# Kernel tuning notes

Measured on AMD Instinct MI355X. Metric: run time of the kernel, lower is better.

Reference implementation:

```python
import jax, jax.numpy as jnp
import numpy as np
import math

B, S, E, H = 4, 2048, 512, 8
D = E // H

def setup_inputs() -> dict:
    key = jax.random.key(0)
    ks = jax.random.split(key, 12)
    inp = {
        'query': jax.random.normal(ks[0], (B, S, E), jnp.float32),
        'key': jax.random.normal(ks[1], (B, S, E), jnp.float32),
        'value': jax.random.normal(ks[2], (B, S, E), jnp.float32),
        'mask': jnp.ones((B, S), jnp.int32),
        'position_bias': jax.random.normal(ks[3], (H, S, S), jnp.float32) * 0.02,
        'Wq': jax.random.normal(ks[4], (E, E), jnp.float32) * 0.02,
        'bq': jnp.zeros((E,), jnp.float32),
        'Wk': jax.random.normal(ks[5], (E, E), jnp.float32) * 0.02,
        'bk': jnp.zeros((E,), jnp.float32),
        'Wv': jax.random.normal(ks[6], (E, E), jnp.float32) * 0.02,
        'bv': jnp.zeros((E,), jnp.float32),
        'Wo': jax.random.normal(ks[7], (E, E), jnp.float32) * 0.02,
        'bo': jnp.zeros((E,), jnp.float32),
    }
    return inp

def reference(query, key, value, mask, position_bias, Wq, bq, Wk, bk, Wv, bv, Wo, bo):
    scale = math.sqrt(D)
    # torch Linear: x @ W.T + b
    Q = (query @ Wq.T + bq).reshape(B, S, H, D).transpose(0, 2, 1, 3)  # bhsd
    K = (key @ Wk.T + bk).reshape(B, S, H, D).transpose(0, 2, 1, 3)
    V = (value @ Wv.T + bv).reshape(B, S, H, D).transpose(0, 2, 1, 3)
    scores = jnp.einsum('bhqd,bhkd->bhqk', Q, K) / scale
    scores = scores + position_bias[None]
    causal = jnp.triu(jnp.ones((S, S), bool), k=1)  # True above diagonal
    scores = jnp.where(causal[None, None], -jnp.inf, scores)
    scores = jnp.where(mask[:, None, None, :] == 0, -jnp.inf, scores)
    attn = jax.nn.softmax(scores, axis=-1)  # dropout is eval no-op
    ctx = jnp.einsum('bhqk,bhkd->bqhd', attn, V).reshape(B, S, E)
    out = ctx @ Wo.T + bo
    return out, attn
```

## Files before the change

### kernel.cpp

```cpp
#include <hip/hip_runtime.h>

typedef __attribute__((ext_vector_type(8))) __bf16 bf16x8;
typedef __attribute__((ext_vector_type(4))) float f32x4;
typedef __attribute__((ext_vector_type(4))) unsigned short u16x4;
typedef unsigned short u16;

#define OFF_QB   0L
#define OFF_KB   4194304L
#define OFF_VB   8388608L
#define OFF_WQ   12582912L
#define OFF_WK   12845056L
#define OFF_WV   13107200L
#define OFF_WO   13369344L
#define OFF_QS   13631488L
#define OFF_KS   17825792L
#define OFF_VT   22020096L
#define OFF_CTX  26214400L
#define WS_NEEDED_U16 30408704L

static __device__ __forceinline__ u16 f2bf(float f) {
  union { float f; unsigned u; } v; v.f = f;
  unsigned r = v.u + 0x7FFFu + ((v.u >> 16) & 1u);
  return (u16)(r >> 16);
}

static __device__ __forceinline__ f32x4 mfma16(bf16x8 a, bf16x8 b, f32x4 c) {
  return __builtin_amdgcn_mfma_f32_16x16x32_bf16(a, b, c, 0, 0, 0);
}

__global__ __launch_bounds__(256) void k_cvt(
    const float* __restrict__ q, const float* __restrict__ k, const float* __restrict__ v,
    const float* __restrict__ wq, const float* __restrict__ wk, const float* __restrict__ wv,
    const float* __restrict__ wo, u16* __restrict__ ws0) {
  long i = ((long)blockIdx.x * 256 + threadIdx.x) * 4;
  const float* src; u16* dst; long off;
  if (i < 12582912L) {
    int which = (int)(i >> 22); off = i & 4194303L;
    src = which == 0 ? q : which == 1 ? k : v;
    dst = ws0 + (long)which * 4194304L;
  } else {
    long j = i - 12582912L;
    int which = (int)(j >> 18); off = j & 262143L;
    src = which == 0 ? wq : which == 1 ? wk : which == 2 ? wv : wo;
    dst = ws0 + 12582912L + (long)which * 262144L;
  }
  float4 f = *(const float4*)(src + off);
  u16x4 o; o.x = f2bf(f.x); o.y = f2bf(f.y); o.z = f2bf(f.z); o.w = f2bf(f.w);
  *(u16x4*)(dst + off) = o;
}

__global__ __launch_bounds__(256) void k_proj_qk(
    const u16* __restrict__ ws0, const float* __restrict__ bq, const float* __restrict__ bk) {
  const int wv  = threadIdx.x >> 6;
  const int lane = threadIdx.x & 63;
  const int r16 = lane & 15, g8 = (lane >> 4) * 8, rq = (lane >> 4) * 4;
  const int t0 = blockIdx.x * 64 + wv * 16;
  const int e0 = blockIdx.y * 64;
  const int z  = blockIdx.z;
  const u16* xb = ws0 + (z == 0 ? OFF_QB : OFF_KB);
  const u16* wb = ws0 + (z == 0 ? OFF_WQ : OFF_WK);
  const float* bias = (z == 0) ? bq : bk;
  u16* dst = (u16*)ws0 + (z == 0 ? OFF_QS : OFF_KS);
  const float scl = (z == 0) ? 0.125f * 1.4426950408889634f : 1.0f;

  f32x4 acc[4] = {};
  const u16* arow = xb + (long)(t0 + r16) * 512 + g8;
  for (int f = 0; f < 512; f += 32) {
    bf16x8 a = *(const bf16x8*)(arow + f);
#pragma unroll
    for (int nt = 0; nt < 4; ++nt) {
      bf16x8 bfr = *(const bf16x8*)(wb + (long)(e0 + nt * 16 + r16) * 512 + f + g8);
      acc[nt] = mfma16(a, bfr, acc[nt]);
    }
  }
#pragma unroll
  for (int nt = 0; nt < 4; ++nt) {
    int e = e0 + nt * 16 + r16;
    float bb = bias[e];
    int h = e >> 6, d = e & 63;
#pragma unroll
    for (int r = 0; r < 4; ++r) {
      int t = t0 + rq + r;
      int b = t >> 11, s = t & 2047;
      float val = (acc[nt][r] + bb) * scl;
      dst[((long)(b * 8 + h) * 2048 + s) * 64 + d] = f2bf(val);
    }
  }
}

__global__ __launch_bounds__(256) void k_proj_v(
    const u16* __restrict__ ws0, const float* __restrict__ bv) {
  const int wv  = threadIdx.x >> 6;
  const int lane = threadIdx.x & 63;
  const int r16 = lane & 15, g8 = (lane >> 4) * 8, rq = (lane >> 4) * 4;
  const int e0 = blockIdx.x * 64 + wv * 16;
  const int t0 = blockIdx.y * 64;
  const u16* xb = ws0 + OFF_VB;
  const u16* wb = ws0 + OFF_WV;
  u16* vt = (u16*)ws0 + OFF_VT;

  f32x4 acc[4] = {};
  const u16* arow = wb + (long)(e0 + r16) * 512 + g8;
  for (int f = 0; f < 512; f += 32) {
    bf16x8 a = *(const bf16x8*)(arow + f);
#pragma unroll
    for (int nt = 0; nt < 4; ++nt) {
      bf16x8 bfr = *(const bf16x8*)(xb + (long)(t0 + nt * 16 + r16) * 512 + f + g8);
      acc[nt] = mfma16(a, bfr, acc[nt]);
    }
  }
#pragma unroll
  for (int r = 0; r < 4; ++r) {
    int e = e0 + rq + r;
    float bb = bv[e];
    int h = e >> 6, d = e & 63;
#pragma unroll
    for (int nt = 0; nt < 4; ++nt) {
      int t = t0 + nt * 16 + r16;
      int b = t >> 11, s = t & 2047;
      vt[((long)((b * 8 + h) * 64 + d)) * 2048 + s] = f2bf(acc[nt][r] + bb);
    }
  }
}

__global__ __launch_bounds__(256) void k_attn(
    const u16* __restrict__ ws0, const float* __restrict__ pos_bias,
    const int* __restrict__ mask, float* __restrict__ attn_out, u16* __restrict__ ctx) {
  __shared__ __align__(16) u16 p_st[4][16][40];
  __shared__ float red_l[4][16];
  __shared__ __align__(16) float cred[4][16][68];

  const int tid = threadIdx.x;
  const int w = tid >> 6, lane = tid & 63;
  const int r16 = lane & 15, g = lane >> 4;
  const int g8 = g * 8, rq = g * 4;
  const int bh = blockIdx.y;
  const int b = bh >> 3, h = bh & 7;
  const int pair = blockIdx.x;
  const u16* Qs = ws0 + OFF_QS + (long)bh * (2048 * 64);
  const u16* Ks = ws0 + OFF_KS + (long)bh * (2048 * 64);
  const u16* VT = ws0 + OFF_VT + (long)bh * (64 * 2048);
  const int* maskb = mask + b * 2048;
  const float NEG = -1e30f;
  const float L2E = 1.4426950408889634f;
  bool dg[4];
#pragma unroll
  for (int r = 0; r < 4; ++r) dg[r] = (r16 > rq + r);

  for (int qsel = 0; qsel < 2; ++qsel) {
    const int qb = qsel ? (127 - pair) : pair;
    const int q0 = qb * 16;
    const int ntiles = qb + 1;
    const int kend = ntiles * 16;
    bf16x8 qf0 = *(const bf16x8*)(Qs + (long)(q0 + r16) * 64 + g8);
    bf16x8 qf1 = *(const bf16x8*)(Qs + (long)(q0 + r16) * 64 + 32 + g8);
    const float* brow = pos_bias + ((long)h * 2048 + q0 + rq) * 2048;

    float l[4] = {0.f, 0.f, 0.f, 0.f};
    for (int ti = w; ti < ntiles; ti += 4) {
      int kcol = ti * 16 + r16;
      bf16x8 kf0 = *(const bf16x8*)(Ks + (long)kcol * 64 + g8);
      bf16x8 kf1 = *(const bf16x8*)(Ks + (long)kcol * 64 + 32 + g8);
      f32x4 s = {};
      s = mfma16(qf0, kf0, s);
      s = mfma16(qf1, kf1, s);
      bool mz = (maskb[kcol] == 0);
      bool edge = (ti == qb);
#pragma unroll
      for (int r = 0; r < 4; ++r) {
        float sv = fmaf(brow[(long)r * 2048 + kcol], L2E, s[r]);
        if (mz || (edge && dg[r])) sv = NEG;
        l[r] += exp2f(sv);
      }
    }
#pragma unroll
    for (int r = 0; r < 4; ++r)
#pragma unroll
      for (int off = 1; off < 16; off <<= 1) l[r] += __shfl_xor(l[r], off);
    if (r16 == 0) {
#pragma unroll
      for (int r = 0; r < 4; ++r) red_l[w][rq + r] = l[r];
    }
    __syncthreads();
    float cc[4];
#pragma unroll
    for (int r = 0; r < 4; ++r) {
      float ls = red_l[0][rq + r] + red_l[1][rq + r] + red_l[2][rq + r] + red_l[3][rq + r];
      cc[r] = -__log2f(ls);
    }

    f32x4 cacc[4] = {};
    float* arow = attn_out + ((long)bh * 2048 + q0) * 2048;
    for (int ta = w; ta < ntiles; ta += 8) {
      const int tb = ta + 4;
      const bool have1 = (tb < ntiles);
      float p0[4], p1[4];
      {
        int kcol = ta * 16 + r16;
        bf16x8 kf0 = *(const bf16x8*)(Ks + (long)kcol * 64 + g8);
        bf16x8 kf1 = *(const bf16x8*)(Ks + (long)kcol * 64 + 32 + g8);
        f32x4 s = {};
        s = mfma16(qf0, kf0, s);
        s = mfma16(qf1, kf1, s);
        bool mz = (maskb[kcol] == 0);
        bool edge = (ta == qb);
#pragma unroll
        for (int r = 0; r < 4; ++r) {
          float sv = fmaf(brow[(long)r * 2048 + kcol], L2E, s[r]);
          if (mz || (edge && dg[r])) sv = NEG;
          float pv = exp2f(sv + cc[r]);
          p0[r] = pv;
          __builtin_nontemporal_store(pv, &arow[(long)(rq + r) * 2048 + kcol]);
        }
      }
      if (have1) {
        int kcol = tb * 16 + r16;
        bf16x8 kf0 = *(const bf16x8*)(Ks + (long)kcol * 64 + g8);
        bf16x8 kf1 = *(const bf16x8*)(Ks + (long)kcol * 64 + 32 + g8);
        f32x4 s = {};
        s = mfma16(qf0, kf0, s);
        s = mfma16(qf1, kf1, s);
        bool mz = (maskb[kcol] == 0);
        bool edge = (tb == qb);
#pragma unroll
        for (int r = 0; r < 4; ++r) {
          float sv = fmaf(brow[(long)r * 2048 + kcol], L2E, s[r]);
          if (mz || (edge && dg[r])) sv = NEG;
          float pv = exp2f(sv + cc[r]);
          p1[r] = pv;
          __builtin_nontemporal_store(pv, &arow[(long)(rq + r) * 2048 + kcol]);
        }
      } else {
#pragma unroll
        for (int r = 0; r < 4; ++r) p1[r] = 0.0f;
      }
#pragma unroll
      for (int r = 0; r < 4; ++r) {
        p_st[w][rq + r][r16]      = f2bf(p0[r]);
        p_st[w][rq + r][16 + r16] = f2bf(p1[r]);
      }
      int tsel = (g < 2) ? ta : (have1 ? tb : ta);
      const u16* vcol = VT + tsel * 16 + (g8 & 15);
      bf16x8 pa = *(const bf16x8*)&p_st[w][r16][g8];
#pragma unroll
      for (int dt = 0; dt < 4; ++dt) {
        bf16x8 vf = *(const bf16x8*)(vcol + (long)(dt * 16 + r16) * 2048);
        cacc[dt] = mfma16(pa, vf, cacc[dt]);
      }
    }
#pragma unroll
    for (int dt = 0; dt < 4; ++dt)
#pragma unroll
      for (int r = 0; r < 4; ++r)
        cred[w][rq + r][dt * 16 + r16] = cacc[dt][r];

    for (int rr = w; rr < 16; rr += 4) {
      float* rowp = arow + (long)rr * 2048;
      for (int k2 = kend + lane * 4; k2 < 2048; k2 += 256) {
        f32x4 z = {0.f, 0.f, 0.f, 0.f};
        __builtin_nontemporal_store(z, (f32x4*)(rowp + k2));
      }
    }
    __syncthreads();
    {
      int row = tid >> 4, c0 = (tid & 15) * 4;
      u16x4 o;
#pragma unroll
      for (int j = 0; j < 4; ++j) {
        float sum = cred[0][row][c0 + j] + cred[1][row][c0 + j] +
                    cred[2][row][c0 + j] + cred[3][row][c0 + j];
        o[j] = f2bf(sum);
      }
      *(u16x4*)&ctx[(long)(b * 2048 + q0 + row) * 512 + h * 64 + c0] = o;
    }
    __syncthreads();
  }
}

__global__ __launch_bounds__(256) void k_oproj(
    const u16* __restrict__ ws0, const float* __restrict__ bo, float* __restrict__ out) {
  const int wv  = threadIdx.x >> 6;
  const int lane = threadIdx.x & 63;
  const int r16 = lane & 15, g8 = (lane >> 4) * 8, rq = (lane >> 4) * 4;
  const int t0 = blockIdx.x * 64 + wv * 16;
  const int e0 = blockIdx.y * 64;
  const u16* ctx = ws0 + OFF_CTX;
  const u16* wb  = ws0 + OFF_WO;
  f32x4 acc[4] = {};
  const u16* arow = ctx + (long)(t0 + r16) * 512 + g8;
  for (int f = 0; f < 512; f += 32) {
    bf16x8 a = *(const bf16x8*)(arow + f);
#pragma unroll
    for (int nt = 0; nt < 4; ++nt) {
      bf16x8 bfr = *(const bf16x8*)(wb + (long)(e0 + nt * 16 + r16) * 512 + f + g8);
      acc[nt] = mfma16(a, bfr, acc[nt]);
    }
  }
#pragma unroll
  for (int nt = 0; nt < 4; ++nt) {
    int e = e0 + nt * 16 + r16;
    float bb = bo[e];
#pragma unroll
    for (int r = 0; r < 4; ++r) {
      out[(long)(t0 + rq + r) * 512 + e] = acc[nt][r] + bb;
    }
  }
}

extern "C" void kernel_launch(void* const* d_in, const int* in_sizes, int n_in,
                              void* d_out, int out_size, void* d_ws, size_t ws_size,
                              hipStream_t stream) {
  if (ws_size < (size_t)WS_NEEDED_U16 * sizeof(u16)) return;
  const float* query = (const float*)d_in[0];
  const float* key   = (const float*)d_in[1];
  const float* value = (const float*)d_in[2];
  const int*   mask  = (const int*)d_in[3];
  const float* pbias = (const float*)d_in[4];
  const float* Wq = (const float*)d_in[5];
  const float* bq = (const float*)d_in[6];
  const float* Wk = (const float*)d_in[7];
  const float* bk = (const float*)d_in[8];
  const float* Wv = (const float*)d_in[9];
  const float* bv = (const float*)d_in[10];
  const float* Wo = (const float*)d_in[11];
  const float* bo = (const float*)d_in[12];
  float* out  = (float*)d_out;
  float* attn = out + 4194304L;
  u16* ws0 = (u16*)d_ws;

  k_cvt<<<13312, 256, 0, stream>>>(query, key, value, Wq, Wk, Wv, Wo, ws0);
  k_proj_qk<<<dim3(128, 8, 2), 256, 0, stream>>>(ws0, bq, bk);
  k_proj_v<<<dim3(8, 128), 256, 0, stream>>>(ws0, bv);
  k_attn<<<dim3(64, 32), 256, 0, stream>>>(ws0, pbias, mask, attn, (u16*)ws0 + OFF_CTX);
  k_oproj<<<dim3(128, 8), 256, 0, stream>>>(ws0, bo, out);
}
```

Before: 429.8 us.

## Make attention single-pass by caching unnormalized probabilities in shared memory

```diff
diff --git a/kernel.cpp b/kernel.cpp
--- a/kernel.cpp
+++ b/kernel.cpp
@@ -3,6 +3,7 @@
 typedef __attribute__((ext_vector_type(8))) __bf16 bf16x8;
 typedef __attribute__((ext_vector_type(4))) float f32x4;
 typedef __attribute__((ext_vector_type(4))) unsigned short u16x4;
+typedef __attribute__((ext_vector_type(8))) unsigned short u16x8;
 typedef unsigned short u16;
 
 #define OFF_QB   0L
@@ -16,7 +17,8 @@
 #define OFF_KS   17825792L
 #define OFF_VT   22020096L
 #define OFF_CTX  26214400L
-#define WS_NEEDED_U16 30408704L
+#define OFF_LWS  30408704L
+#define WS_NEEDED_U16 30932992L
 
 static __device__ __forceinline__ u16 f2bf(float f) {
   union { float f; unsigned u; } v; v.f = f;
@@ -24,8 +26,16 @@
   return (u16)(r >> 16);
 }
 
+static __device__ __forceinline__ float bf2f(u16 x) {
+  union { unsigned u; float f; } v; v.u = ((unsigned)x) << 16; return v.f;
+}
+
 static __device__ __forceinline__ f32x4 mfma16(bf16x8 a, bf16x8 b, f32x4 c) {
   return __builtin_amdgcn_mfma_f32_16x16x32_bf16(a, b, c, 0, 0, 0);
+}
+
+static __device__ __forceinline__ int swz(int row, int col) {
+  return ((row << 11) + col) ^ ((row & 7) << 3);
 }
 
 __global__ __launch_bounds__(256) void k_cvt(
@@ -125,10 +135,10 @@
 
 __global__ __launch_bounds__(256) void k_attn(
     const u16* __restrict__ ws0, const float* __restrict__ pos_bias,
-    const int* __restrict__ mask, float* __restrict__ attn_out, u16* __restrict__ ctx) {
-  __shared__ __align__(16) u16 p_st[4][16][40];
-  __shared__ float red_l[4][16];
-  __shared__ __align__(16) float cred[4][16][68];
+    const int* __restrict__ mask, float* __restrict__ attn_out, u16* __restrict__ ctx,
+    float* __restrict__ lws) {
+  __shared__ __align__(16) unsigned char smem[65536];
+  u16* pL = (u16*)smem;
 
   const int tid = threadIdx.x;
   const int w = tid >> 6, lane = tid & 63;
@@ -136,144 +146,132 @@
   const int g8 = g * 8, rq = g * 4;
   const int bh = blockIdx.y;
   const int b = bh >> 3, h = bh & 7;
-  const int pair = blockIdx.x;
+  const int qb = 127 - blockIdx.x;
+  const int q0 = qb * 16;
+  const int ntiles = qb + 1;
   const u16* Qs = ws0 + OFF_QS + (long)bh * (2048 * 64);
   const u16* Ks = ws0 + OFF_KS + (long)bh * (2048 * 64);
   const u16* VT = ws0 + OFF_VT + (long)bh * (64 * 2048);
   const int* maskb = mask + b * 2048;
+  float* lw = lws + ((long)bh * 128 + blockIdx.x) * 64;
   const float NEG = -1e30f;
   const float L2E = 1.4426950408889634f;
   bool dg[4];
 #pragma unroll
   for (int r = 0; r < 4; ++r) dg[r] = (r16 > rq + r);
 
-  for (int qsel = 0; qsel < 2; ++qsel) {
-    const int qb = qsel ? (127 - pair) : pair;
-    const int q0 = qb * 16;
-    const int ntiles = qb + 1;
-    const int kend = ntiles * 16;
-    bf16x8 qf0 = *(const bf16x8*)(Qs + (long)(q0 + r16) * 64 + g8);
-    bf16x8 qf1 = *(const bf16x8*)(Qs + (long)(q0 + r16) * 64 + 32 + g8);
-    const float* brow = pos_bias + ((long)h * 2048 + q0 + rq) * 2048;
-
-    float l[4] = {0.f, 0.f, 0.f, 0.f};
-    for (int ti = w; ti < ntiles; ti += 4) {
-      int kcol = ti * 16 + r16;
+  bf16x8 qf0 = *(const bf16x8*)(Qs + (long)(q0 + r16) * 64 + g8);
+  bf16x8 qf1 = *(const bf16x8*)(Qs + (long)(q0 + r16) * 64 + 32 + g8);
+  const float* brow = pos_bias + ((long)h * 2048 + q0 + rq) * 2048;
+
+  float l[4] = {0.f, 0.f, 0.f, 0.f};
+  f32x4 cacc[4] = {};
+  for (int ta = 2 * w; ta < ntiles; ta += 8) {
+    const int tb = ta + 1;
+    const bool have1 = (tb < ntiles);
+    {
+      int kcol = ta * 16 + r16;
       bf16x8 kf0 = *(const bf16x8*)(Ks + (long)kcol * 64 + g8);
       bf16x8 kf1 = *(const bf16x8*)(Ks + (long)kcol * 64 + 32 + g8);
       f32x4 s = {};
       s = mfma16(qf0, kf0, s);
       s = mfma16(qf1, kf1, s);
       bool mz = (maskb[kcol] == 0);
-      bool edge = (ti == qb);
+      bool edge = (ta == qb);
 #pragma unroll
       for (int r = 0; r < 4; ++r) {
         float sv = fmaf(brow[(long)r * 2048 + kcol], L2E, s[r]);
         if (mz || (edge && dg[r])) sv = NEG;
-        l[r] += exp2f(sv);
+        float p = exp2f(sv);
+        l[r] += p;
+        pL[swz(rq + r, kcol)] = f2bf(p);
       }
     }
-#pragma unroll
-    for (int r = 0; r < 4; ++r)
-#pragma unroll
-      for (int off = 1; off < 16; off <<= 1) l[r] += __shfl_xor(l[r], off);
-    if (r16 == 0) {
-#pragma unroll
-      for (int r = 0; r < 4; ++r) red_l[w][rq + r] = l[r];
-    }
-    __syncthreads();
-    float cc[4];
-#pragma unroll
-    for (int r = 0; r < 4; ++r) {
-      float ls = red_l[0][rq + r] + red_l[1][rq + r] + red_l[2][rq + r] + red_l[3][rq + r];
-      cc[r] = -__log2f(ls);
-    }
-
-    f32x4 cacc[4] = {};
-    float* arow = attn_out + ((long)bh * 2048 + q0) * 2048;
-    for (int ta = w; ta < ntiles; ta += 8) {
-      const int tb = ta + 4;
-      const bool have1 = (tb < ntiles);
-      float p0[4], p1[4];
-      {
-        int kcol = ta * 16 + r16;
-        bf16x8 kf0 = *(const bf16x8*)(Ks + (long)kcol * 64 + g8);
-        bf16x8 kf1 = *(const bf16x8*)(Ks + (long)kcol * 64 + 32 + g8);
-        f32x4 s = {};
-        s = mfma16(qf0, kf0, s);
-        s = mfma16(qf1, kf1, s);
-        bool mz = (maskb[kcol] == 0);
-        bool edge = (ta == qb);
-#pragma unroll
-        for (int r = 0; r < 4; ++r) {
-          float sv = fmaf(brow[(long)r * 2048 + kcol], L2E, s[r]);
-          if (mz || (edge && dg[r])) sv = NEG;
-          float pv = exp2f(sv + cc[r]);
-          p0[r] = pv;
-          __builtin_nontemporal_store(pv, &arow[(long)(rq + r) * 2048 + kcol]);
-        }
+    if (have1) {
+      int kcol = tb * 16 + r16;
+      bf16x8 kf0 = *(const bf16x8*)(Ks + (long)kcol * 64 + g8);
+      bf16x8 kf1 = *(const bf16x8*)(Ks + (long)kcol * 64 + 32 + g8);
+      f32x4 s = {};
+      s = mfma16(qf0, kf0, s);
+      s = mfma16(qf1, kf1, s);
+      bool mz = (maskb[kcol] == 0);
+      bool edge = (tb == qb);
+#pragma unroll
+      for (int r = 0; r < 4; ++r) {
+        float sv = fmaf(brow[(long)r * 2048 + kcol], L2E, s[r]);
+        if (mz || (edge && dg[r])) sv = NEG;
+        float p = exp2f(sv);
+        l[r] += p;
+        pL[swz(rq + r, kcol)] = f2bf(p);
       }
-      if (have1) {
-        int kcol = tb * 16 + r16;
-        bf16x8 kf0 = *(const bf16x8*)(Ks + (long)kcol * 64 + g8);
-        bf16x8 kf1 = *(const bf16x8*)(Ks + (long)kcol * 64 + 32 + g8);
-        f32x4 s = {};
-        s = mfma16(qf0, kf0, s);
-        s = mfma16(qf1, kf1, s);
-        bool mz = (maskb[kcol] == 0);
-        bool edge = (tb == qb);
-#pragma unroll
-        for (int r = 0; r < 4; ++r) {
-          float sv = fmaf(brow[(long)r * 2048 + kcol], L2E, s[r]);
-          if (mz || (edge && dg[r])) sv = NEG;
-          float pv = exp2f(sv + cc[r]);
-          p1[r] = pv;
-          __builtin_nontemporal_store(pv, &arow[(long)(rq + r) * 2048 + kcol]);
-        }
-      } else {
-#pragma unroll
-        for (int r = 0; r < 4; ++r) p1[r] = 0.0f;
-      }
-#pragma unroll
-      for (int r = 0; r < 4; ++r) {
-        p_st[w][rq + r][r16]      = f2bf(p0[r]);
-        p_st[w][rq + r][16 + r16] = f2bf(p1[r]);
-      }
-      int tsel = (g < 2) ? ta : (have1 ? tb : ta);
-      const u16* vcol = VT + tsel * 16 + (g8 & 15);
-      bf16x8 pa = *(const bf16x8*)&p_st[w][r16][g8];
+    } else {
+#pragma unroll
+      for (int r = 0; r < 4; ++r) pL[swz(rq + r, tb * 16 + r16)] = 0;
+    }
+    {
+      bf16x8 pa = *(const bf16x8*)&pL[swz(r16, ta * 16 + g8)];
+      const u16* vcol = VT + ta * 16 + g8;
 #pragma unroll
       for (int dt = 0; dt < 4; ++dt) {
         bf16x8 vf = *(const bf16x8*)(vcol + (long)(dt * 16 + r16) * 2048);
         cacc[dt] = mfma16(pa, vf, cacc[dt]);
       }
     }
-#pragma unroll
-    for (int dt = 0; dt < 4; ++dt)
-#pragma unroll
-      for (int r = 0; r < 4; ++r)
-        cred[w][rq + r][dt * 16 + r16] = cacc[dt][r];
-
-    for (int rr = w; rr < 16; rr += 4) {
-      float* rowp = arow + (long)rr * 2048;
-      for (int k2 = kend + lane * 4; k2 < 2048; k2 += 256) {
-        f32x4 z = {0.f, 0.f, 0.f, 0.f};
-        __builtin_nontemporal_store(z, (f32x4*)(rowp + k2));
+  }
+#pragma unroll
+  for (int r = 0; r < 4; ++r)
+#pragma unroll
+    for (int off = 1; off < 16; off <<= 1) l[r] += __shfl_xor(l[r], off);
+  if (r16 == 0) {
+#pragma unroll
+    for (int r = 0; r < 4; ++r) lw[w * 16 + rq + r] = l[r];
+  }
+  __threadfence();
+  __syncthreads();
+
+  const int wrow = lane >> 2;
+  float ls = lw[wrow] + lw[16 + wrow] + lw[32 + wrow] + lw[48 + wrow];
+  float il = 1.0f / ls;
+  const int kend_pad = ((ntiles + 1) & ~1) * 16;
+  float* arow = attn_out + ((long)bh * 2048 + q0) * 2048;
+  for (int c = w * 32 + (lane & 3) * 8; c < 2048; c += 128) {
+    float* dp = arow + (long)wrow * 2048 + c;
+    f32x4 v0, v1;
+    if (c < kend_pad) {
+      u16x8 pb = *(const u16x8*)&pL[swz(wrow, c)];
+#pragma unroll
+      for (int j = 0; j < 4; ++j) {
+        v0[j] = bf2f(pb[j]) * il;
+        v1[j] = bf2f(pb[4 + j]) * il;
       }
-    }
-    __syncthreads();
-    {
-      int row = tid >> 4, c0 = (tid & 15) * 4;
-      u16x4 o;
-#pragma unroll
-      for (int j = 0; j < 4; ++j) {
-        float sum = cred[0][row][c0 + j] + cred[1][row][c0 + j] +
-                    cred[2][row][c0 + j] + cred[3][row][c0 + j];
-        o[j] = f2bf(sum);
-      }
-      *(u16x4*)&ctx[(long)(b * 2048 + q0 + row) * 512 + h * 64 + c0] = o;
-    }
-    __syncthreads();
+    } else {
+      v0 = (f32x4){0.f, 0.f, 0.f, 0.f};
+      v1 = (f32x4){0.f, 0.f, 0.f, 0.f};
+    }
+    __builtin_nontemporal_store(v0, (f32x4*)dp);
+    __builtin_nontemporal_store(v1, (f32x4*)(dp + 4));
+  }
+  __syncthreads();
+
+  float* credf = (float*)smem;
+#pragma unroll
+  for (int dt = 0; dt < 4; ++dt)
+#pragma unroll
+    for (int r = 0; r < 4; ++r)
+      credf[(w * 16 + rq + r) * 68 + dt * 16 + r16] = cacc[dt][r];
+  __syncthreads();
+  {
+    int row = tid >> 4, c0 = (tid & 15) * 4;
+    float ls2 = lw[row] + lw[16 + row] + lw[32 + row] + lw[48 + row];
+    float il2 = 1.0f / ls2;
+    u16x4 o;
+#pragma unroll
+    for (int j = 0; j < 4; ++j) {
+      float sum = credf[(0 + row) * 68 + c0 + j] + credf[(16 + row) * 68 + c0 + j] +
+                  credf[(32 + row) * 68 + c0 + j] + credf[(48 + row) * 68 + c0 + j];
+      o[j] = f2bf(sum * il2);
+    }
+    *(u16x4*)&ctx[(long)(b * 2048 + q0 + row) * 512 + h * 64 + c0] = o;
   }
 }
 
@@ -331,6 +329,8 @@
   k_cvt<<<13312, 256, 0, stream>>>(query, key, value, Wq, Wk, Wv, Wo, ws0);
   k_proj_qk<<<dim3(128, 8, 2), 256, 0, stream>>>(ws0, bq, bk);
   k_proj_v<<<dim3(8, 128), 256, 0, stream>>>(ws0, bv);
-  k_attn<<<dim3(64, 32), 256, 0, stream>>>(ws0, pbias, mask, attn, (u16*)ws0 + OFF_CTX);
+  k_attn<<<dim3(128, 32), 256, 0, stream>>>(ws0, pbias, mask, attn,
+                                            (u16*)ws0 + OFF_CTX,
+                                            (float*)((u16*)d_ws + OFF_LWS));
   k_oproj<<<dim3(128, 8), 256, 0, stream>>>(ws0, bo, out);
 }
```

Result: slower. 1.393 ms (+224.0%).
